# Performance work log

Hardware: AMD Instinct MI355X
Metric: run time of the kernel (lower is better)

Reference implementation:

```python
import jax, jax.numpy as jnp
import numpy as np

EPS = 1e-5

def conv1d(x, w, b):
    # x: (N,C,L), w: (O,I,3), stride 1, padding 1 -> same length
    y = jax.lax.conv_general_dilated(x, w, window_strides=(1,), padding=((1, 1),),
                                     dimension_numbers=('NCH', 'OIH', 'NCH'))
    return y + b[None, :, None]

def bn(x, g, b):
    # BatchNorm1d, training-mode batch statistics over (N, L) per channel
    m = x.mean(axis=(0, 2), keepdims=True)
    v = x.var(axis=(0, 2), keepdims=True)
    return (x - m) * jax.lax.rsqrt(v + EPS) * g[None, :, None] + b[None, :, None]

def setup_inputs() -> dict:
    V, E, H, L, NL = 50257, 512, 512, 2048, 2
    D = 1 + NL * 2  # 5 channels in the pre-attention conv stack
    key = jax.random.key(0)
    ks = iter(jax.random.split(key, 48))
    def rn(shape, s=0.02):
        return jax.random.normal(next(ks), shape, dtype=jnp.float32) * s
    inp = dict(
        emb=rn((V, E), 1.0),
        conv1_w=rn((32, D, 3)), conv1_b=rn((32,)),
        conv2_w=rn((D, 32, 3)), conv2_b=rn((D,)),
        conv3_w=rn((1, D, 3)), conv3_b=rn((1,)),
        conv4_w=rn((32, 3, 3)), conv4_b=rn((32,)),
        conv5_w=rn((3, 32, 3)), conv5_b=rn((3,)),
        conv6_w=rn((1, 3, 3)), conv6_b=rn((1,)),
        bn1_g=jnp.ones((32,)), bn1_b=jnp.zeros((32,)),
        bn2_g=jnp.ones((D,)), bn2_b=jnp.zeros((D,)),
        bn3_g=jnp.ones((1,)), bn3_b=jnp.zeros((1,)),
        bn4_g=jnp.ones((32,)), bn4_b=jnp.zeros((32,)),
        bn5_g=jnp.ones((3,)), bn5_b=jnp.zeros((3,)),
        bn6_g=jnp.ones((1,)), bn6_b=jnp.zeros((1,)),
        att_w=rn((L, E)), att_b=rn((L,)),
        gru_wih=rn((4, 3 * H, E)), gru_whh=rn((4, 3 * H, H)),
        gru_bih=rn((4, 3 * H)), gru_bhh=rn((4, 3 * H)),
        lo_w=rn((V, H)), lo_b=rn((V,)),
        h_state=rn((4, 1, H), 1.0),
        encoder_outs=rn((L, 2 * H), 1.0),
        x=jax.random.randint(next(ks), (1,), 0, V),
    )
    return inp

def reference(emb, conv1_w, conv1_b, conv2_w, conv2_b, conv3_w, conv3_b,
              conv4_w, conv4_b, conv5_w, conv5_b, conv6_w, conv6_b,
              bn1_g, bn1_b, bn2_g, bn2_b, bn3_g, bn3_b,
              bn4_g, bn4_b, bn5_g, bn5_b, bn6_g, bn6_b,
              att_w, att_b, gru_wih, gru_whh, gru_bih, gru_bhh,
              lo_w, lo_b, h_state, encoder_outs, x):
    H = h_state.shape[-1]
    # dropout(p=0.1) treated as identity (eval mode / deterministic reference)
    embadded = emb[x].reshape(1, 1, H)                                      # (1,1,512)
    pre = jnp.concatenate([h_state.reshape(1, -1, H), embadded], axis=1)    # (1,5,512)
    c = jax.nn.relu(bn(conv1d(pre, conv1_w, conv1_b), bn1_g, bn1_b))        # (1,32,512)
    pre = jax.nn.relu(bn(conv1d(c, conv2_w, conv2_b) + pre, bn2_g, bn2_b))  # residual, (1,5,512)
    pre = jax.nn.relu(bn(conv1d(pre, conv3_w, conv3_b), bn3_g, bn3_b))      # (1,1,512)
    aw = jax.nn.softmax(pre.reshape(1, -1) @ att_w.T + att_b, axis=1)       # (1,L)
    app = (aw @ encoder_outs).reshape(1, -1, H)                             # (1,2,512) (bidir encoder)
    com = jnp.concatenate([app, embadded], axis=1)                          # (1,3,512)
    c = jax.nn.relu(bn(conv1d(com, conv4_w, conv4_b), bn4_g, bn4_b))        # (1,32,512)
    com = jax.nn.relu(bn(conv1d(c, conv5_w, conv5_b) + com, bn5_g, bn5_b))  # residual, (1,3,512)
    com = jax.nn.relu(bn(conv1d(com, conv6_w, conv6_b), bn6_g, bn6_b))      # (1,1,512)
    # 4-layer stacked GRU, single time step, batch 1 (PyTorch gate order r,z,n)
    xt = com.reshape(H)
    h_new = []
    for l in range(h_state.shape[0]):
        gi = gru_wih[l] @ xt + gru_bih[l]
        gh = gru_whh[l] @ h_state[l, 0] + gru_bhh[l]
        ir, iz, inn = jnp.split(gi, 3)
        hr, hz, hn = jnp.split(gh, 3)
        r = jax.nn.sigmoid(ir + hr)
        z = jax.nn.sigmoid(iz + hz)
        n = jnp.tanh(inn + r * hn)
        xt = (1.0 - z) * n + z * h_state[l, 0]
        h_new.append(xt)
    h_state_new = jnp.stack(h_new)[:, None, :]                              # (4,1,512)
    out = jax.nn.log_softmax((xt @ lo_w.T + lo_b)[None, :], axis=1)         # (1,V)
    return out, h_state_new
```

## Files before the change

kernel.cpp:

```cpp
#include <hip/hip_runtime.h>
#include <hip/hip_bf16.h>

typedef __attribute__((ext_vector_type(4))) float f32x4;

constexpr int WSF_PRE1 = 0;
constexpr int WSF_LOGA = 512;
constexpr int WSF_PART = 2560;
constexpr int WSF_SUME = 18944;
constexpr int WSF_XT   = 18960;
constexpr int WSF_LOGV = 21520;
constexpr int WSF_PM   = 71792;
constexpr int WSF_PS   = 72592;
constexpr int WSF_LSE  = 73392;
constexpr int NVOCAB   = 50257;
constexpr int NBLK_V   = 786;

__device__ __forceinline__ float wave_rsum(float v) {
#pragma unroll
    for (int o = 32; o > 0; o >>= 1) v += __shfl_down(v, o);
    return v;
}
__device__ __forceinline__ float sigm(float x) { return 1.0f / (1.0f + __expf(-x)); }

__global__ __launch_bounds__(512) void k_pre(
    const float* __restrict__ emb, const int* __restrict__ xidx,
    const float* __restrict__ hstate,
    const float* __restrict__ w1, const float* __restrict__ b1,
    const float* __restrict__ w2, const float* __restrict__ b2,
    const float* __restrict__ w3, const float* __restrict__ b3,
    const float* __restrict__ g1, const float* __restrict__ bb1,
    const float* __restrict__ g2, const float* __restrict__ bb2,
    const float* __restrict__ g3, const float* __restrict__ bb3,
    float* __restrict__ ws)
{
    constexpr int W1 = 0, B1 = 480, G1 = 512, BB1 = 544;
    constexpr int W2 = 576, B2 = 1056, G2 = 1061, BB2 = 1066;
    constexpr int W3 = 1071, B3 = 1086, G3 = 1087, BB3 = 1088, NW = 1089;
    __shared__ float s_w[NW];
    __shared__ float s_pre[5][512];
    __shared__ float s_y[32][512];
    __shared__ float s_stat[32][2];

    const int tid = threadIdx.x;
    const int lane = tid & 63, wid = tid >> 6;
    const int l = tid;

    if (tid < 480) s_w[W1 + tid] = w1[tid];
    if (tid < 32) { s_w[B1 + tid] = b1[tid]; s_w[G1 + tid] = g1[tid]; s_w[BB1 + tid] = bb1[tid]; }
    if (tid < 480) s_w[W2 + tid] = w2[tid];
    if (tid < 5) { s_w[B2 + tid] = b2[tid]; s_w[G2 + tid] = g2[tid]; s_w[BB2 + tid] = bb2[tid]; }
    if (tid < 15) s_w[W3 + tid] = w3[tid];
    if (tid == 0) { s_w[B3] = b3[0]; s_w[G3] = g3[0]; s_w[BB3] = bb3[0]; }

    const int x = xidx[0];
#pragma unroll
    for (int c = 0; c < 4; ++c) s_pre[c][l] = hstate[c * 512 + l];
    s_pre[4][l] = emb[(size_t)x * 512 + l];
    __syncthreads();

    float px[5][3];
#pragma unroll
    for (int ic = 0; ic < 5; ++ic) {
        px[ic][0] = (l > 0)   ? s_pre[ic][l - 1] : 0.0f;
        px[ic][1] =             s_pre[ic][l];
        px[ic][2] = (l < 511) ? s_pre[ic][l + 1] : 0.0f;
    }
#pragma unroll 4
    for (int oc = 0; oc < 32; ++oc) {
        float a = s_w[B1 + oc];
#pragma unroll
        for (int ic = 0; ic < 5; ++ic)
#pragma unroll
            for (int k = 0; k < 3; ++k)
                a += s_w[W1 + oc * 15 + ic * 3 + k] * px[ic][k];
        s_y[oc][l] = a;
    }
    __syncthreads();

#pragma unroll
    for (int t = 0; t < 4; ++t) {
        const int oc = wid * 4 + t;
        float s = 0.f, s2 = 0.f;
#pragma unroll
        for (int j = 0; j < 8; ++j) {
            float v = s_y[oc][lane + j * 64];
            s += v; s2 += v * v;
        }
        s = wave_rsum(s); s2 = wave_rsum(s2);
        if (lane == 0) {
            float m = s * (1.0f / 512.0f);
            float var = s2 * (1.0f / 512.0f) - m * m;
            s_stat[oc][0] = m; s_stat[oc][1] = rsqrtf(var + 1e-5f);
        }
    }
    __syncthreads();

#pragma unroll 4
    for (int oc = 0; oc < 32; ++oc) {
        float m = s_stat[oc][0], r = s_stat[oc][1];
        s_y[oc][l] = fmaxf((s_y[oc][l] - m) * r * s_w[G1 + oc] + s_w[BB1 + oc], 0.0f);
    }
    __syncthreads();

    float y2[5];
#pragma unroll
    for (int oc = 0; oc < 5; ++oc) y2[oc] = s_w[B2 + oc];
#pragma unroll 2
    for (int ic = 0; ic < 32; ++ic) {
        float c0 = (l > 0)   ? s_y[ic][l - 1] : 0.0f;
        float c1 =             s_y[ic][l];
        float c2 = (l < 511) ? s_y[ic][l + 1] : 0.0f;
#pragma unroll
        for (int oc = 0; oc < 5; ++oc) {
            const int base = W2 + (oc * 32 + ic) * 3;
            y2[oc] += s_w[base] * c0 + s_w[base + 1] * c1 + s_w[base + 2] * c2;
        }
    }
#pragma unroll
    for (int oc = 0; oc < 5; ++oc) y2[oc] += s_pre[oc][l];
    __syncthreads();
#pragma unroll
    for (int oc = 0; oc < 5; ++oc) s_y[oc][l] = y2[oc];
    __syncthreads();

    if (wid < 5) {
        const int oc = wid;
        float s = 0.f, s2 = 0.f;
#pragma unroll
        for (int j = 0; j < 8; ++j) {
            float v = s_y[oc][lane + j * 64];
            s += v; s2 += v * v;
        }
        s = wave_rsum(s); s2 = wave_rsum(s2);
        if (lane == 0) {
            float m = s * (1.0f / 512.0f);
            float var = s2 * (1.0f / 512.0f) - m * m;
            s_stat[oc][0] = m; s_stat[oc][1] = rsqrtf(var + 1e-5f);
        }
    }
    __syncthreads();
#pragma unroll
    for (int oc = 0; oc < 5; ++oc) {
        float m = s_stat[oc][0], r = s_stat[oc][1];
        s_pre[oc][l] = fmaxf((y2[oc] - m) * r * s_w[G2 + oc] + s_w[BB2 + oc], 0.0f);
    }
    __syncthreads();

    float a3 = s_w[B3];
#pragma unroll
    for (int ic = 0; ic < 5; ++ic) {
        float c0 = (l > 0)   ? s_pre[ic][l - 1] : 0.0f;
        float c1 =             s_pre[ic][l];
        float c2 = (l < 511) ? s_pre[ic][l + 1] : 0.0f;
        a3 += s_w[W3 + ic * 3] * c0 + s_w[W3 + ic * 3 + 1] * c1 + s_w[W3 + ic * 3 + 2] * c2;
    }
    s_y[0][l] = a3;
    __syncthreads();
    if (wid == 0) {
        float s = 0.f, s2 = 0.f;
#pragma unroll
        for (int j = 0; j < 8; ++j) {
            float v = s_y[0][lane + j * 64];
            s += v; s2 += v * v;
        }
        s = wave_rsum(s); s2 = wave_rsum(s2);
        if (lane == 0) {
            float m = s * (1.0f / 512.0f);
            float var = s2 * (1.0f / 512.0f) - m * m;
            s_stat[0][0] = m; s_stat[0][1] = rsqrtf(var + 1e-5f);
        }
    }
    __syncthreads();
    ws[WSF_PRE1 + l] = fmaxf((a3 - s_stat[0][0]) * s_stat[0][1] * s_w[G3] + s_w[BB3], 0.0f);
}

__global__ __launch_bounds__(256) void k_attlogit(
    const float* __restrict__ attw, const float* __restrict__ attb,
    float* __restrict__ ws)
{
    const int tid = threadIdx.x, lane = tid & 63, wid = tid >> 6;
    float q0[4], q1[4];
#pragma unroll
    for (int j = 0; j < 4; ++j) {
        q0[j] = ws[WSF_PRE1 + lane * 4 + j];
        q1[j] = ws[WSF_PRE1 + 256 + lane * 4 + j];
    }
    const int row0 = (blockIdx.x * 4 + wid) * 4;
#pragma unroll
    for (int r = 0; r < 4; ++r) {
        const int row = row0 + r;
        f32x4 w0 = *reinterpret_cast<const f32x4*>(attw + (size_t)row * 512 + lane * 4);
        f32x4 w1 = *reinterpret_cast<const f32x4*>(attw + (size_t)row * 512 + 256 + lane * 4);
        float a = 0.f;
#pragma unroll
        for (int j = 0; j < 4; ++j) a += w0[j] * q0[j] + w1[j] * q1[j];
        a = wave_rsum(a);
        if (lane == 0) ws[WSF_LOGA + row] = a + attb[row];
    }
}

__global__ __launch_bounds__(256) void k_attpv(
    const float* __restrict__ enc, float* __restrict__ ws)
{
    __shared__ float s_e[2048];
    __shared__ float s_r[256];
    const int tid = threadIdx.x;
#pragma unroll
    for (int k = 0; k < 8; ++k) s_e[tid + k * 256] = ws[WSF_LOGA + tid + k * 256];
    __syncthreads();
    float m = -INFINITY;
#pragma unroll
    for (int k = 0; k < 8; ++k) m = fmaxf(m, s_e[tid + k * 256]);
    s_r[tid] = m; __syncthreads();
    for (int s = 128; s > 0; s >>= 1) {
        if (tid < s) s_r[tid] = fmaxf(s_r[tid], s_r[tid + s]);
        __syncthreads();
    }
    const float M = s_r[0];
    __syncthreads();
    float t = 0.f;
#pragma unroll
    for (int k = 0; k < 8; ++k) {
        const int i = tid + k * 256;
        float e = __expf(s_e[i] - M);
        s_e[i] = e;
        t += e;
    }
    s_r[tid] = t; __syncthreads();
    for (int s = 128; s > 0; s >>= 1) {
        if (tid < s) s_r[tid] += s_r[tid + s];
        __syncthreads();
    }
    const float S = s_r[0];
    if (blockIdx.x == 0 && tid == 0) ws[WSF_SUME] = S;

    const int jc = blockIdx.x >> 1, half = blockIdx.x & 1;
    const int col = half * 512 + tid * 2;
    const float* ep = enc + (size_t)(jc * 128) * 1024 + col;
    float a0 = 0.f, a1 = 0.f;
#pragma unroll 4
    for (int jj = 0; jj < 128; ++jj) {
        const float w = s_e[jc * 128 + jj];
        float2 e = *reinterpret_cast<const float2*>(ep + (size_t)jj * 1024);
        a0 += w * e.x;
        a1 += w * e.y;
    }
    ws[WSF_PART + jc * 1024 + col]     = a0;
    ws[WSF_PART + jc * 1024 + col + 1] = a1;
}

__global__ __launch_bounds__(512) void k_post(
    const float* __restrict__ emb, const int* __restrict__ xidx,
    const float* __restrict__ w4, const float* __restrict__ b4,
    const float* __restrict__ w5, const float* __restrict__ b5,
    const float* __restrict__ w6, const float* __restrict__ b6,
    const float* __restrict__ g4, const float* __restrict__ bb4,
    const float* __restrict__ g5, const float* __restrict__ bb5,
    const float* __restrict__ g6, const float* __restrict__ bb6,
    float* __restrict__ ws)
{
    constexpr int W4 = 0, B4 = 288, G4 = 320, BB4 = 352;
    constexpr int W5 = 384, B5 = 672, G5 = 675, BB5 = 678;
    constexpr int W6 = 681, B6 = 690, G6 = 691, BB6 = 692, NW = 693;
    __shared__ float s_w[NW];
    __shared__ float s_com[3][512];
    __shared__ float s_y[32][512];
    __shared__ float s_stat[32][2];

    const int tid = threadIdx.x;
    const int lane = tid & 63, wid = tid >> 6;
    const int l = tid;

    if (tid < 288) s_w[W4 + tid] = w4[tid];
    if (tid < 32) { s_w[B4 + tid] = b4[tid]; s_w[G4 + tid] = g4[tid]; s_w[BB4 + tid] = bb4[tid]; }
    if (tid < 288) s_w[W5 + tid] = w5[tid];
    if (tid < 3) { s_w[B5 + tid] = b5[tid]; s_w[G5 + tid] = g5[tid]; s_w[BB5 + tid] = bb5[tid]; }
    if (tid < 9) s_w[W6 + tid] = w6[tid];
    if (tid == 0) { s_w[B6] = b6[0]; s_w[G6] = g6[0]; s_w[BB6] = bb6[0]; }

    const float invS = 1.0f / ws[WSF_SUME];
    float a0 = 0.f, a1 = 0.f;
#pragma unroll
    for (int p = 0; p < 16; ++p) {
        a0 += ws[WSF_PART + p * 1024 + l];
        a1 += ws[WSF_PART + p * 1024 + 512 + l];
    }
    const int x = xidx[0];
    s_com[0][l] = a0 * invS;
    s_com[1][l] = a1 * invS;
    s_com[2][l] = emb[(size_t)x * 512 + l];
    __syncthreads();

    float px[3][3];
#pragma unroll
    for (int ic = 0; ic < 3; ++ic) {
        px[ic][0] = (l > 0)   ? s_com[ic][l - 1] : 0.0f;
        px[ic][1] =             s_com[ic][l];
        px[ic][2] = (l < 511) ? s_com[ic][l + 1] : 0.0f;
    }
#pragma unroll 4
    for (int oc = 0; oc < 32; ++oc) {
        float a = s_w[B4 + oc];
#pragma unroll
        for (int ic = 0; ic < 3; ++ic)
#pragma unroll
            for (int k = 0; k < 3; ++k)
                a += s_w[W4 + oc * 9 + ic * 3 + k] * px[ic][k];
        s_y[oc][l] = a;
    }
    __syncthreads();

#pragma unroll
    for (int t = 0; t < 4; ++t) {
        const int oc = wid * 4 + t;
        float s = 0.f, s2 = 0.f;
#pragma unroll
        for (int j = 0; j < 8; ++j) {
            float v = s_y[oc][lane + j * 64];
            s += v; s2 += v * v;
        }
        s = wave_rsum(s); s2 = wave_rsum(s2);
        if (lane == 0) {
            float m = s * (1.0f / 512.0f);
            float var = s2 * (1.0f / 512.0f) - m * m;
            s_stat[oc][0] = m; s_stat[oc][1] = rsqrtf(var + 1e-5f);
        }
    }
    __syncthreads();
#pragma unroll 4
    for (int oc = 0; oc < 32; ++oc) {
        float m = s_stat[oc][0], r = s_stat[oc][1];
        s_y[oc][l] = fmaxf((s_y[oc][l] - m) * r * s_w[G4 + oc] + s_w[BB4 + oc], 0.0f);
    }
    __syncthreads();

    float y2[3];
#pragma unroll
    for (int oc = 0; oc < 3; ++oc) y2[oc] = s_w[B5 + oc];
#pragma unroll 2
    for (int ic = 0; ic < 32; ++ic) {
        float c0 = (l > 0)   ? s_y[ic][l - 1] : 0.0f;
        float c1 =             s_y[ic][l];
        float c2 = (l < 511) ? s_y[ic][l + 1] : 0.0f;
#pragma unroll
        for (int oc = 0; oc < 3; ++oc) {
            const int base = W5 + (oc * 32 + ic) * 3;
            y2[oc] += s_w[base] * c0 + s_w[base + 1] * c1 + s_w[base + 2] * c2;
        }
    }
#pragma unroll
    for (int oc = 0; oc < 3; ++oc) y2[oc] += s_com[oc][l];
    __syncthreads();
#pragma unroll
    for (int oc = 0; oc < 3; ++oc) s_y[oc][l] = y2[oc];
    __syncthreads();
    if (wid < 3) {
        const int oc = wid;
        float s = 0.f, s2 = 0.f;
#pragma unroll
        for (int j = 0; j < 8; ++j) {
            float v = s_y[oc][lane + j * 64];
            s += v; s2 += v * v;
        }
        s = wave_rsum(s); s2 = wave_rsum(s2);
        if (lane == 0) {
            float m = s * (1.0f / 512.0f);
            float var = s2 * (1.0f / 512.0f) - m * m;
            s_stat[oc][0] = m; s_stat[oc][1] = rsqrtf(var + 1e-5f);
        }
    }
    __syncthreads();
#pragma unroll
    for (int oc = 0; oc < 3; ++oc) {
        float m = s_stat[oc][0], r = s_stat[oc][1];
        s_com[oc][l] = fmaxf((y2[oc] - m) * r * s_w[G5 + oc] + s_w[BB5 + oc], 0.0f);
    }
    __syncthreads();

    float a6 = s_w[B6];
#pragma unroll
    for (int ic = 0; ic < 3; ++ic) {
        float c0 = (l > 0)   ? s_com[ic][l - 1] : 0.0f;
        float c1 =             s_com[ic][l];
        float c2 = (l < 511) ? s_com[ic][l + 1] : 0.0f;
        a6 += s_w[W6 + ic * 3] * c0 + s_w[W6 + ic * 3 + 1] * c1 + s_w[W6 + ic * 3 + 2] * c2;
    }
    s_y[0][l] = a6;
    __syncthreads();
    if (wid == 0) {
        float s = 0.f, s2 = 0.f;
#pragma unroll
        for (int j = 0; j < 8; ++j) {
            float v = s_y[0][lane + j * 64];
            s += v; s2 += v * v;
        }
        s = wave_rsum(s); s2 = wave_rsum(s2);
        if (lane == 0) {
            float m = s * (1.0f / 512.0f);
            float var = s2 * (1.0f / 512.0f) - m * m;
            s_stat[0][0] = m; s_stat[0][1] = rsqrtf(var + 1e-5f);
        }
    }
    __syncthreads();
    ws[WSF_XT + l] = fmaxf((a6 - s_stat[0][0]) * s_stat[0][1] * s_w[G6] + s_w[BB6], 0.0f);
}

__global__ __launch_bounds__(256) void k_gru(
    const float* __restrict__ wih, const float* __restrict__ whh,
    const float* __restrict__ bih, const float* __restrict__ bhh,
    const float* __restrict__ hstate,
    const float* __restrict__ xt_in, float* __restrict__ xt_out,
    float* __restrict__ hout, int layer)
{
    wih += (size_t)layer * 1536 * 512;
    whh += (size_t)layer * 1536 * 512;
    bih += layer * 1536;
    bhh += layer * 1536;
    const float* hp = hstate + layer * 512;

    const int tid = threadIdx.x, lane = tid & 63, wid = tid >> 6;
    float xq0[4], xq1[4], hq0[4], hq1[4];
#pragma unroll
    for (int j = 0; j < 4; ++j) {
        xq0[j] = xt_in[lane * 4 + j];
        xq1[j] = xt_in[256 + lane * 4 + j];
        hq0[j] = hp[lane * 4 + j];
        hq1[j] = hp[256 + lane * 4 + j];
    }
    __shared__ float s_g[8][6];
    const int i0 = blockIdx.x * 8;
#pragma unroll
    for (int t = 0; t < 2; ++t) {
        const int ii = wid * 2 + t;
        const int i = i0 + ii;
        float a[6] = {0.f, 0.f, 0.f, 0.f, 0.f, 0.f};
#pragma unroll
        for (int g = 0; g < 3; ++g) {
            const float* wr = wih + (size_t)(i + g * 512) * 512;
            f32x4 w0 = *reinterpret_cast<const f32x4*>(wr + lane * 4);
            f32x4 w1 = *reinterpret_cast<const f32x4*>(wr + 256 + lane * 4);
#pragma unroll
            for (int j = 0; j < 4; ++j) a[g] += w0[j] * xq0[j] + w1[j] * xq1[j];
        }
#pragma unroll
        for (int g = 0; g < 3; ++g) {
            const float* wr = whh + (size_t)(i + g * 512) * 512;
            f32x4 w0 = *reinterpret_cast<const f32x4*>(wr + lane * 4);
            f32x4 w1 = *reinterpret_cast<const f32x4*>(wr + 256 + lane * 4);
#pragma unroll
            for (int j = 0; j < 4; ++j) a[3 + g] += w0[j] * hq0[j] + w1[j] * hq1[j];
        }
#pragma unroll
        for (int g = 0; g < 6; ++g) a[g] = wave_rsum(a[g]);
        if (lane == 0) {
#pragma unroll
            for (int g = 0; g < 6; ++g) s_g[ii][g] = a[g];
        }
    }
    __syncthreads();
    if (tid < 8) {
        const int i = i0 + tid;
        float ir = s_g[tid][0] + bih[i];
        float iz = s_g[tid][1] + bih[i + 512];
        float in_ = s_g[tid][2] + bih[i + 1024];
        float hr = s_g[tid][3] + bhh[i];
        float hz = s_g[tid][4] + bhh[i + 512];
        float hn = s_g[tid][5] + bhh[i + 1024];
        float r = sigm(ir + hr);
        float z = sigm(iz + hz);
        float n = tanhf(in_ + r * hn);
        float hprev = hp[i];
        float h = (1.0f - z) * n + z * hprev;
        xt_out[i] = h;
        hout[i] = h;
    }
}

__global__ __launch_bounds__(256) void k_vocab(
    const float* __restrict__ low, const float* __restrict__ lob,
    float* __restrict__ ws)
{
    const int tid = threadIdx.x, lane = tid & 63, wid = tid >> 6;
    float q0[4], q1[4];
#pragma unroll
    for (int j = 0; j < 4; ++j) {
        q0[j] = ws[WSF_XT + 4 * 512 + lane * 4 + j];
        q1[j] = ws[WSF_XT + 4 * 512 + 256 + lane * 4 + j];
    }

    const int row0 = blockIdx.x * 64 + wid * 16;
    float m = -INFINITY, s = 0.0f;
#pragma unroll 4
    for (int r = 0; r < 16; ++r) {
        const int row = row0 + r;
        if (row < NVOCAB) {
            f32x4 w0 = *reinterpret_cast<const f32x4*>(low + (size_t)row * 512 + lane * 4);
            f32x4 w1 = *reinterpret_cast<const f32x4*>(low + (size_t)row * 512 + 256 + lane * 4);
            float a = 0.f;
#pragma unroll
            for (int j = 0; j < 4; ++j) a += w0[j] * q0[j] + w1[j] * q1[j];
            a = wave_rsum(a);
            if (lane == 0) {
                float v = a + lob[row];
                ws[WSF_LOGV + row] = v;
                if (v > m) { s = s * __expf(m - v) + 1.0f; m = v; }
                else       { s += __expf(v - m); }
            }
        }
    }
    __shared__ float sm[4], ss[4];
    if (lane == 0) { sm[wid] = m; ss[wid] = s; }
    __syncthreads();
    if (tid == 0) {
        float M = -INFINITY, S = 0.0f;
#pragma unroll
        for (int w = 0; w < 4; ++w) {
            float mb = sm[w], sb = ss[w];
            if (sb > 0.0f) {
                if (mb > M) { S = S * __expf(M - mb) + sb; M = mb; }
                else        { S += sb * __expf(mb - M); }
            }
        }
        ws[WSF_PM + blockIdx.x] = M;
        ws[WSF_PS + blockIdx.x] = S;
    }
}

__global__ __launch_bounds__(256) void k_lse(float* __restrict__ ws, int nb)
{
    __shared__ float sm[256], ss[256];
    const int tid = threadIdx.x;
    float M = -INFINITY, S = 0.0f;
    for (int i = tid; i < nb; i += 256) {
        float mb = ws[WSF_PM + i], sb = ws[WSF_PS + i];
        if (sb > 0.0f) {
            if (mb > M) { S = S * __expf(M - mb) + sb; M = mb; }
            else        { S += sb * __expf(mb - M); }
        }
    }
    sm[tid] = M; ss[tid] = S;
    __syncthreads();
    for (int st = 128; st > 0; st >>= 1) {
        if (tid < st) {
            float mb = sm[tid + st], sb = ss[tid + st];
            if (sb > 0.0f) {
                if (mb > sm[tid]) { ss[tid] = ss[tid] * __expf(sm[tid] - mb) + sb; sm[tid] = mb; }
                else              { ss[tid] += sb * __expf(mb - sm[tid]); }
            }
        }
        __syncthreads();
    }
    if (tid == 0) ws[WSF_LSE] = sm[0] + logf(ss[0]);
}

__global__ __launch_bounds__(256) void k_out(
    const float* __restrict__ ws, float* __restrict__ out)
{
    const int i = blockIdx.x * 256 + threadIdx.x;
    if (i < NVOCAB) out[i] = ws[WSF_LOGV + i] - ws[WSF_LSE];
}

extern "C" void kernel_launch(void* const* d_in, const int* in_sizes, int n_in,
                              void* d_out, int out_size, void* d_ws, size_t ws_size,
                              hipStream_t stream)
{
    (void)in_sizes; (void)n_in; (void)out_size; (void)ws_size;
    const float* emb     = (const float*)d_in[0];
    const float* conv1_w = (const float*)d_in[1];  const float* conv1_b = (const float*)d_in[2];
    const float* conv2_w = (const float*)d_in[3];  const float* conv2_b = (const float*)d_in[4];
    const float* conv3_w = (const float*)d_in[5];  const float* conv3_b = (const float*)d_in[6];
    const float* conv4_w = (const float*)d_in[7];  const float* conv4_b = (const float*)d_in[8];
    const float* conv5_w = (const float*)d_in[9];  const float* conv5_b = (const float*)d_in[10];
    const float* conv6_w = (const float*)d_in[11]; const float* conv6_b = (const float*)d_in[12];
    const float* bn1_g = (const float*)d_in[13];   const float* bn1_b = (const float*)d_in[14];
    const float* bn2_g = (const float*)d_in[15];   const float* bn2_b = (const float*)d_in[16];
    const float* bn3_g = (const float*)d_in[17];   const float* bn3_b = (const float*)d_in[18];
    const float* bn4_g = (const float*)d_in[19];   const float* bn4_b = (const float*)d_in[20];
    const float* bn5_g = (const float*)d_in[21];   const float* bn5_b = (const float*)d_in[22];
    const float* bn6_g = (const float*)d_in[23];   const float* bn6_b = (const float*)d_in[24];
    const float* att_w = (const float*)d_in[25];   const float* att_b = (const float*)d_in[26];
    const float* gru_wih = (const float*)d_in[27]; const float* gru_whh = (const float*)d_in[28];
    const float* gru_bih = (const float*)d_in[29]; const float* gru_bhh = (const float*)d_in[30];
    const float* lo_w = (const float*)d_in[31];    const float* lo_b = (const float*)d_in[32];
    const float* h_state = (const float*)d_in[33];
    const float* enc = (const float*)d_in[34];
    const int* x = (const int*)d_in[35];

    float* ws = (float*)d_ws;
    float* out = (float*)d_out;

    k_pre<<<1, 512, 0, stream>>>(emb, x, h_state,
        conv1_w, conv1_b, conv2_w, conv2_b, conv3_w, conv3_b,
        bn1_g, bn1_b, bn2_g, bn2_b, bn3_g, bn3_b, ws);
    k_attlogit<<<128, 256, 0, stream>>>(att_w, att_b, ws);
    k_attpv<<<32, 256, 0, stream>>>(enc, ws);
    k_post<<<1, 512, 0, stream>>>(emb, x,
        conv4_w, conv4_b, conv5_w, conv5_b, conv6_w, conv6_b,
        bn4_g, bn4_b, bn5_g, bn5_b, bn6_g, bn6_b, ws);
    for (int l = 0; l < 4; ++l) {
        k_gru<<<64, 256, 0, stream>>>(gru_wih, gru_whh, gru_bih, gru_bhh, h_state,
            ws + WSF_XT + l * 512, ws + WSF_XT + (l + 1) * 512,
            out + NVOCAB + l * 512, l);
    }
    k_vocab<<<NBLK_V, 256, 0, stream>>>(lo_w, lo_b, ws);
    k_lse<<<1, 256, 0, stream>>>(ws, NBLK_V);
    k_out<<<197, 256, 0, stream>>>(ws, out);
}
```

Measured before the change: 100.4 us.

## Hoist GRU hidden matvecs off critical path and split attention softmax across blocks

Computes all four layers' W_hh·h products up front in one wide kernel, since they depend only on the input hidden state. The per-layer GRU kernel then only does the input matvec, with twice as many blocks. Attention logits now emit per-block max and sum partials, so the attention-weighting kernel no longer redoes a full 2048-element softmax reduction in every block. That kernel also runs with more blocks over shorter chunks. The log-sum-exp and output subtraction are fused into one kernel, which removes a launch but has every block redo the 786-partial reduction.

```diff
diff --git a/kernel.cpp b/kernel.cpp
--- a/kernel.cpp
+++ b/kernel.cpp
@@ -5,13 +5,14 @@
 
 constexpr int WSF_PRE1 = 0;
 constexpr int WSF_LOGA = 512;
-constexpr int WSF_PART = 2560;
-constexpr int WSF_SUME = 18944;
-constexpr int WSF_XT   = 18960;
-constexpr int WSF_LOGV = 21520;
-constexpr int WSF_PM   = 71792;
-constexpr int WSF_PS   = 72592;
-constexpr int WSF_LSE  = 73392;
+constexpr int WSF_ATTM = 2560;
+constexpr int WSF_ATTS = 2688;
+constexpr int WSF_PART = 2816;
+constexpr int WSF_XT   = 35584;
+constexpr int WSF_GH   = 38144;
+constexpr int WSF_LOGV = 44288;
+constexpr int WSF_PM   = 94560;
+constexpr int WSF_PS   = 95360;
 constexpr int NVOCAB   = 50257;
 constexpr int NBLK_V   = 786;
 
@@ -21,6 +22,31 @@
     return v;
 }
 __device__ __forceinline__ float sigm(float x) { return 1.0f / (1.0f + __expf(-x)); }
+
+__global__ __launch_bounds__(256) void k_gruh(
+    const float* __restrict__ whh, const float* __restrict__ bhh,
+    const float* __restrict__ hstate, float* __restrict__ ws)
+{
+    const int tid = threadIdx.x, lane = tid & 63, wid = tid >> 6;
+    const int R = blockIdx.x * 4 + wid;
+    const int l = R / 1536;
+    const int r = R - l * 1536;
+    const float* hp = hstate + l * 512;
+    float h0[4], h1[4];
+#pragma unroll
+    for (int j = 0; j < 4; ++j) {
+        h0[j] = hp[lane * 4 + j];
+        h1[j] = hp[256 + lane * 4 + j];
+    }
+    const float* wr = whh + ((size_t)l * 1536 + r) * 512;
+    f32x4 w0 = *reinterpret_cast<const f32x4*>(wr + lane * 4);
+    f32x4 w1 = *reinterpret_cast<const f32x4*>(wr + 256 + lane * 4);
+    float a = 0.f;
+#pragma unroll
+    for (int j = 0; j < 4; ++j) a += w0[j] * h0[j] + w1[j] * h1[j];
+    a = wave_rsum(a);
+    if (lane == 0) ws[WSF_GH + R] = a + bhh[l * 1536 + r];
+}
 
 __global__ __launch_bounds__(512) void k_pre(
     const float* __restrict__ emb, const int* __restrict__ xidx,
@@ -94,7 +120,6 @@
         }
     }
     __syncthreads();
-
 #pragma unroll 4
     for (int oc = 0; oc < 32; ++oc) {
         float m = s_stat[oc][0], r = s_stat[oc][1];
@@ -178,6 +203,7 @@
     const float* __restrict__ attw, const float* __restrict__ attb,
     float* __restrict__ ws)
 {
+    __shared__ float s_l[16];
     const int tid = threadIdx.x, lane = tid & 63, wid = tid >> 6;
     float q0[4], q1[4];
 #pragma unroll
@@ -195,55 +221,48 @@
 #pragma unroll
         for (int j = 0; j < 4; ++j) a += w0[j] * q0[j] + w1[j] * q1[j];
         a = wave_rsum(a);
-        if (lane == 0) ws[WSF_LOGA + row] = a + attb[row];
+        if (lane == 0) {
+            float v = a + attb[row];
+            ws[WSF_LOGA + row] = v;
+            s_l[wid * 4 + r] = v;
+        }
+    }
+    __syncthreads();
+    if (tid == 0) {
+        float m = -INFINITY;
+#pragma unroll
+        for (int k = 0; k < 16; ++k) m = fmaxf(m, s_l[k]);
+        float s = 0.f;
+#pragma unroll
+        for (int k = 0; k < 16; ++k) s += __expf(s_l[k] - m);
+        ws[WSF_ATTM + blockIdx.x] = m;
+        ws[WSF_ATTS + blockIdx.x] = s;
     }
 }
 
 __global__ __launch_bounds__(256) void k_attpv(
     const float* __restrict__ enc, float* __restrict__ ws)
 {
-    __shared__ float s_e[2048];
-    __shared__ float s_r[256];
     const int tid = threadIdx.x;
-#pragma unroll
-    for (int k = 0; k < 8; ++k) s_e[tid + k * 256] = ws[WSF_LOGA + tid + k * 256];
-    __syncthreads();
-    float m = -INFINITY;
-#pragma unroll
-    for (int k = 0; k < 8; ++k) m = fmaxf(m, s_e[tid + k * 256]);
-    s_r[tid] = m; __syncthreads();
-    for (int s = 128; s > 0; s >>= 1) {
-        if (tid < s) s_r[tid] = fmaxf(s_r[tid], s_r[tid + s]);
-        __syncthreads();
-    }
-    const float M = s_r[0];
-    __syncthreads();
-    float t = 0.f;
-#pragma unroll
-    for (int k = 0; k < 8; ++k) {
-        const int i = tid + k * 256;
-        float e = __expf(s_e[i] - M);
-        s_e[i] = e;
-        t += e;
-    }
-    s_r[tid] = t; __syncthreads();
-    for (int s = 128; s > 0; s >>= 1) {
-        if (tid < s) s_r[tid] += s_r[tid + s];
-        __syncthreads();
-    }
-    const float S = s_r[0];
-    if (blockIdx.x == 0 && tid == 0) ws[WSF_SUME] = S;
-
+    float M = -INFINITY, S = 0.f;
+    for (int i = 0; i < 128; ++i) {
+        float mb = ws[WSF_ATTM + i], sb = ws[WSF_ATTS + i];
+        if (mb > M) { S = S * __expf(M - mb) + sb; M = mb; }
+        else        { S += sb * __expf(mb - M); }
+    }
     const int jc = blockIdx.x >> 1, half = blockIdx.x & 1;
+    __shared__ float s_e[64];
+    if (tid < 64) s_e[tid] = __expf(ws[WSF_LOGA + jc * 64 + tid] - M);
+    __syncthreads();
+
     const int col = half * 512 + tid * 2;
-    const float* ep = enc + (size_t)(jc * 128) * 1024 + col;
+    const float* ep = enc + (size_t)(jc * 64) * 1024 + col;
     float a0 = 0.f, a1 = 0.f;
 #pragma unroll 4
-    for (int jj = 0; jj < 128; ++jj) {
-        const float w = s_e[jc * 128 + jj];
+    for (int jj = 0; jj < 64; ++jj) {
         float2 e = *reinterpret_cast<const float2*>(ep + (size_t)jj * 1024);
-        a0 += w * e.x;
-        a1 += w * e.y;
+        a0 += s_e[jj] * e.x;
+        a1 += s_e[jj] * e.y;
     }
     ws[WSF_PART + jc * 1024 + col]     = a0;
     ws[WSF_PART + jc * 1024 + col + 1] = a1;
@@ -278,10 +297,16 @@
     if (tid < 9) s_w[W6 + tid] = w6[tid];
     if (tid == 0) { s_w[B6] = b6[0]; s_w[G6] = g6[0]; s_w[BB6] = bb6[0]; }
 
-    const float invS = 1.0f / ws[WSF_SUME];
+    float M = -INFINITY, S = 0.f;
+    for (int i = 0; i < 128; ++i) {
+        float mb = ws[WSF_ATTM + i], sb = ws[WSF_ATTS + i];
+        if (mb > M) { S = S * __expf(M - mb) + sb; M = mb; }
+        else        { S += sb * __expf(mb - M); }
+    }
+    const float invS = 1.0f / S;
     float a0 = 0.f, a1 = 0.f;
-#pragma unroll
-    for (int p = 0; p < 16; ++p) {
+#pragma unroll 8
+    for (int p = 0; p < 32; ++p) {
         a0 += ws[WSF_PART + p * 1024 + l];
         a1 += ws[WSF_PART + p * 1024 + 512 + l];
     }
@@ -405,72 +430,43 @@
     ws[WSF_XT + l] = fmaxf((a6 - s_stat[0][0]) * s_stat[0][1] * s_w[G6] + s_w[BB6], 0.0f);
 }
 
-__global__ __launch_bounds__(256) void k_gru(
-    const float* __restrict__ wih, const float* __restrict__ whh,
-    const float* __restrict__ bih, const float* __restrict__ bhh,
+__global__ __launch_bounds__(256) void k_grux(
+    const float* __restrict__ wih, const float* __restrict__ bih,
     const float* __restrict__ hstate,
     const float* __restrict__ xt_in, float* __restrict__ xt_out,
-    float* __restrict__ hout, int layer)
+    float* __restrict__ hout, const float* __restrict__ gh, int layer)
 {
     wih += (size_t)layer * 1536 * 512;
-    whh += (size_t)layer * 1536 * 512;
     bih += layer * 1536;
-    bhh += layer * 1536;
     const float* hp = hstate + layer * 512;
 
     const int tid = threadIdx.x, lane = tid & 63, wid = tid >> 6;
-    float xq0[4], xq1[4], hq0[4], hq1[4];
+    float xq0[4], xq1[4];
 #pragma unroll
     for (int j = 0; j < 4; ++j) {
         xq0[j] = xt_in[lane * 4 + j];
         xq1[j] = xt_in[256 + lane * 4 + j];
-        hq0[j] = hp[lane * 4 + j];
-        hq1[j] = hp[256 + lane * 4 + j];
-    }
-    __shared__ float s_g[8][6];
-    const int i0 = blockIdx.x * 8;
-#pragma unroll
-    for (int t = 0; t < 2; ++t) {
-        const int ii = wid * 2 + t;
-        const int i = i0 + ii;
-        float a[6] = {0.f, 0.f, 0.f, 0.f, 0.f, 0.f};
-#pragma unroll
-        for (int g = 0; g < 3; ++g) {
-            const float* wr = wih + (size_t)(i + g * 512) * 512;
-            f32x4 w0 = *reinterpret_cast<const f32x4*>(wr + lane * 4);
-            f32x4 w1 = *reinterpret_cast<const f32x4*>(wr + 256 + lane * 4);
-#pragma unroll
-            for (int j = 0; j < 4; ++j) a[g] += w0[j] * xq0[j] + w1[j] * xq1[j];
-        }
-#pragma unroll
-        for (int g = 0; g < 3; ++g) {
-            const float* wr = whh + (size_t)(i + g * 512) * 512;
-            f32x4 w0 = *reinterpret_cast<const f32x4*>(wr + lane * 4);
-            f32x4 w1 = *reinterpret_cast<const f32x4*>(wr + 256 + lane * 4);
-#pragma unroll
-            for (int j = 0; j < 4; ++j) a[3 + g] += w0[j] * hq0[j] + w1[j] * hq1[j];
-        }
-#pragma unroll
-        for (int g = 0; g < 6; ++g) a[g] = wave_rsum(a[g]);
-        if (lane == 0) {
-#pragma unroll
-            for (int g = 0; g < 6; ++g) s_g[ii][g] = a[g];
-        }
-    }
-    __syncthreads();
-    if (tid < 8) {
-        const int i = i0 + tid;
-        float ir = s_g[tid][0] + bih[i];
-        float iz = s_g[tid][1] + bih[i + 512];
-        float in_ = s_g[tid][2] + bih[i + 1024];
-        float hr = s_g[tid][3] + bhh[i];
-        float hz = s_g[tid][4] + bhh[i + 512];
-        float hn = s_g[tid][5] + bhh[i + 1024];
-        float r = sigm(ir + hr);
-        float z = sigm(iz + hz);
-        float n = tanhf(in_ + r * hn);
-        float hprev = hp[i];
-        float h = (1.0f - z) * n + z * hprev;
+    }
+    __shared__ float s_g[4][3];
+    const int u = blockIdx.x * 4 + wid;
+#pragma unroll
+    for (int g = 0; g < 3; ++g) {
+        const float* wr = wih + (size_t)(u + g * 512) * 512;
+        f32x4 w0 = *reinterpret_cast<const f32x4*>(wr + lane * 4);
+        f32x4 w1 = *reinterpret_cast<const f32x4*>(wr + 256 + lane * 4);
+        float a = 0.f;
+#pragma unroll
+        for (int j = 0; j < 4; ++j) a += w0[j] * xq0[j] + w1[j] * xq1[j];
+        a = wave_rsum(a);
+        if (lane == 0) s_g[wid][g] = a + bih[u + g * 512];
+    }
+    __syncthreads();
+    if (tid < 4) {
+        const int i = blockIdx.x * 4 + tid;
+        float r = sigm(s_g[tid][0] + gh[i]);
+        float z = sigm(s_g[tid][1] + gh[i + 512]);
+        float n = tanhf(s_g[tid][2] + r * gh[i + 1024]);
+        float h = (1.0f - z) * n + z * hp[i];
         xt_out[i] = h;
         hout[i] = h;
     }
@@ -526,17 +522,16 @@
     }
 }
 
-__global__ __launch_bounds__(256) void k_lse(float* __restrict__ ws, int nb)
+__global__ __launch_bounds__(256) void k_outlse(
+    const float* __restrict__ ws, float* __restrict__ out)
 {
     __shared__ float sm[256], ss[256];
     const int tid = threadIdx.x;
     float M = -INFINITY, S = 0.0f;
-    for (int i = tid; i < nb; i += 256) {
+    for (int i = tid; i < NBLK_V; i += 256) {
         float mb = ws[WSF_PM + i], sb = ws[WSF_PS + i];
-        if (sb > 0.0f) {
-            if (mb > M) { S = S * __expf(M - mb) + sb; M = mb; }
-            else        { S += sb * __expf(mb - M); }
-        }
+        if (mb > M) { S = S * __expf(M - mb) + sb; M = mb; }
+        else        { S += sb * __expf(mb - M); }
     }
     sm[tid] = M; ss[tid] = S;
     __syncthreads();
@@ -550,14 +545,9 @@
         }
         __syncthreads();
     }
-    if (tid == 0) ws[WSF_LSE] = sm[0] + logf(ss[0]);
-}
-
-__global__ __launch_bounds__(256) void k_out(
-    const float* __restrict__ ws, float* __restrict__ out)
-{
-    const int i = blockIdx.x * 256 + threadIdx.x;
-    if (i < NVOCAB) out[i] = ws[WSF_LOGV + i] - ws[WSF_LSE];
+    const float lse = sm[0] + logf(ss[0]);
+    const int i = blockIdx.x * 256 + tid;
+    if (i < NVOCAB) out[i] = ws[WSF_LOGV + i] - lse;
 }
 
 extern "C" void kernel_launch(void* const* d_in, const int* in_sizes, int n_in,
@@ -589,20 +579,20 @@
     float* ws = (float*)d_ws;
     float* out = (float*)d_out;
 
+    k_gruh<<<1536, 256, 0, stream>>>(gru_whh, gru_bhh, h_state, ws);
     k_pre<<<1, 512, 0, stream>>>(emb, x, h_state,
         conv1_w, conv1_b, conv2_w, conv2_b, conv3_w, conv3_b,
         bn1_g, bn1_b, bn2_g, bn2_b, bn3_g, bn3_b, ws);
     k_attlogit<<<128, 256, 0, stream>>>(att_w, att_b, ws);
-    k_attpv<<<32, 256, 0, stream>>>(enc, ws);
+    k_attpv<<<64, 256, 0, stream>>>(enc, ws);
     k_post<<<1, 512, 0, stream>>>(emb, x,
         conv4_w, conv4_b, conv5_w, conv5_b, conv6_w, conv6_b,
         bn4_g, bn4_b, bn5_g, bn5_b, bn6_g, bn6_b, ws);
     for (int l = 0; l < 4; ++l) {
-        k_gru<<<64, 256, 0, stream>>>(gru_wih, gru_whh, gru_bih, gru_bhh, h_state,
+        k_grux<<<128, 256, 0, stream>>>(gru_wih, gru_bih, h_state,
             ws + WSF_XT + l * 512, ws + WSF_XT + (l + 1) * 512,
-            out + NVOCAB + l * 512, l);
+            out + NVOCAB + l * 512, ws + WSF_GH + l * 1536, l);
     }
     k_vocab<<<NBLK_V, 256, 0, stream>>>(lo_w, lo_b, ws);
-    k_lse<<<1, 256, 0, stream>>>(ws, NBLK_V);
-    k_out<<<197, 256, 0, stream>>>(ws, out);
-}
+    k_outlse<<<197, 256, 0, stream>>>(ws, out);
+}
```

Result: slower. 112.2 us (+11.8%).
